# Performance work log

Measured on AMD Instinct MI355X. Metric: run time of the kernel, lower is better.

Reference implementation:

```python
import jax, jax.numpy as jnp
import numpy as np

H, KV, D = 12, 2, 128        # q heads, kv heads, head_dim
HID = 1536
B, S = 4, 2048               # equal-length packed sequences
T = B * S
EPS = 1e-6
ROPE_THETA = 10000.0


def _rms_norm(x, w):
    # RMSNorm over last dim in fp32, as in Qwen3RMSNorm
    xf = x.astype(jnp.float32)
    var = jnp.mean(xf * xf, axis=-1, keepdims=True)
    return (w * (xf * jax.lax.rsqrt(var + EPS))).astype(x.dtype)


def _apply_rope(x, cos, sin):
    # x: [T, h, D]; cos/sin: [T, D/2] -> expand over heads
    half = cos.shape[-1]
    x1, x2 = x[..., :half], x[..., half:2 * half]
    c = cos[:, None, :]
    s = sin[:, None, :]
    return jnp.concatenate([x1 * c - x2 * s, x1 * s + x2 * c], axis=-1)


def setup_inputs() -> dict:
    key = jax.random.key(0)
    ks = jax.random.split(key, 8)
    hidden_states = jax.random.normal(ks[0], (T, HID), dtype=jnp.float32)
    # real RoPE tables over per-sequence positions
    inv_freq = 1.0 / (ROPE_THETA ** (np.arange(0, D, 2, dtype=np.float32) / D))  # [D/2]
    pos = np.tile(np.arange(S, dtype=np.float32), B)                              # [T]
    ang = pos[:, None] * inv_freq[None, :]
    cos = jnp.asarray(np.cos(ang), dtype=jnp.float32)
    sin = jnp.asarray(np.sin(ang), dtype=jnp.float32)
    sc = 0.02
    Wq = jax.random.normal(ks[1], (HID, H * D), dtype=jnp.float32) * sc
    Wk = jax.random.normal(ks[2], (HID, KV * D), dtype=jnp.float32) * sc
    Wv = jax.random.normal(ks[3], (HID, KV * D), dtype=jnp.float32) * sc
    Wo = jax.random.normal(ks[4], (H * D, HID), dtype=jnp.float32) * sc
    q_norm_w = jnp.ones((D,), dtype=jnp.float32)
    k_norm_w = jnp.ones((D,), dtype=jnp.float32)
    cu_seqlens = jnp.arange(B + 1, dtype=jnp.int32) * S
    return {"hidden_states": hidden_states, "cos": cos, "sin": sin,
            "Wq": Wq, "Wk": Wk, "Wv": Wv, "Wo": Wo,
            "q_norm_w": q_norm_w, "k_norm_w": k_norm_w,
            "cu_seqlens": cu_seqlens}


def reference(hidden_states, cos, sin, Wq, Wk, Wv, Wo, q_norm_w, k_norm_w, cu_seqlens):
    # QKV projections on packed tokens
    q = (hidden_states @ Wq).reshape(T, H, D)
    k = (hidden_states @ Wk).reshape(T, KV, D)
    v = (hidden_states @ Wv).reshape(T, KV, D)
    # Qwen3 per-head QK RMSNorm, then RoPE
    q = _apply_rope(_rms_norm(q, q_norm_w), cos, sin)
    k = _apply_rope(_rms_norm(k, k_norm_w), cos, sin)
    # equal-length sequences: unpack to [B, h, S, D] (block-diagonal varlen attn)
    qb = q.reshape(B, S, H, D).transpose(0, 2, 1, 3)
    kb = k.reshape(B, S, KV, D).transpose(0, 2, 1, 3)
    vb = v.reshape(B, S, KV, D).transpose(0, 2, 1, 3)
    # GQA: repeat kv heads
    rep = H // KV
    kb = jnp.repeat(kb, rep, axis=1)
    vb = jnp.repeat(vb, rep, axis=1)
    scale = D ** -0.5
    scores = jnp.einsum('bhqd,bhkd->bhqk', qb, kb) * scale
    causal = jnp.tril(jnp.ones((S, S), dtype=bool))
    scores = jnp.where(causal[None, None], scores, jnp.finfo(scores.dtype).min)
    attn = jax.nn.softmax(scores, axis=-1)
    out = jnp.einsum('bhqk,bhkd->bhqd', attn, vb)       # [B,H,S,D]
    out = out.transpose(0, 2, 1, 3).reshape(T, H * D)   # repack
    return out @ Wo
```

## Files before the change

kernel.cpp:

```cpp
#include <hip/hip_runtime.h>
#include <hip/hip_bf16.h>
#include <stdint.h>

#define H_   12
#define KV_  2
#define D_   128
#define HID_ 1536
#define B_   4
#define S_   2048
#define T_   (B_*S_)

typedef __attribute__((ext_vector_type(8))) short  bf16x8;
typedef __attribute__((ext_vector_type(4))) float  f32x4;

__device__ __forceinline__ ushort f2bf(float f) {
  union { float f; uint32_t u; } v; v.f = f;
  uint32_t u = v.u;
  return (ushort)((u + 0x7fffu + ((u >> 16) & 1u)) >> 16);
}
__device__ __forceinline__ float bf2f(ushort u) {
  union { uint32_t u; float f; } v; v.u = ((uint32_t)u) << 16;
  return v.f;
}
__device__ __forceinline__ uint32_t cvtpk_bf16(float lo, float hi) {
  uint32_t r;
  asm("v_cvt_pk_bf16_f32 %0, %1, %2" : "=v"(r) : "v"(lo), "v"(hi));
  return r;
}

__device__ __forceinline__ void gload_lds16(const void* g, void* l) {
  __builtin_amdgcn_global_load_lds(
      (const __attribute__((address_space(1))) uint32_t*)g,
      (__attribute__((address_space(3))) uint32_t*)l, 16, 0, 0);
}

__global__ __launch_bounds__(256) void cvt_f32_bf16(const float* __restrict__ in,
                                                    ushort* __restrict__ out, int n) {
  int i = (blockIdx.x * 256 + threadIdx.x) * 4;
  if (i + 3 < n) {
    float4 v = *(const float4*)&in[i];
    ushort4 o;
    o.x = f2bf(v.x); o.y = f2bf(v.y); o.z = f2bf(v.z); o.w = f2bf(v.w);
    *(ushort4*)&out[i] = o;
  }
}

__global__ __launch_bounds__(256) void transpose_cvt2(const float* __restrict__ W0,
                                                      ushort* __restrict__ Wt0,
                                                      const float* __restrict__ W1,
                                                      ushort* __restrict__ Wt1,
                                                      int K, int N) {
  __shared__ float tile[32][33];
  const float* W  = blockIdx.z ? W1  : W0;
  ushort*      Wt = blockIdx.z ? Wt1 : Wt0;
  int k0 = blockIdx.x * 32, n0 = blockIdx.y * 32;
  int tx = threadIdx.x & 31, ty = threadIdx.x >> 5;
#pragma unroll
  for (int i = 0; i < 32; i += 8)
    tile[ty + i][tx] = W[(long)(k0 + ty + i) * N + n0 + tx];
  __syncthreads();
#pragma unroll
  for (int i = 0; i < 32; i += 8)
    Wt[(long)(n0 + ty + i) * K + k0 + tx] = f2bf(tile[tx][ty + i]);
}

template <int OUT_F32>
__global__ __launch_bounds__(256, 2) void gemm_bt(const ushort* __restrict__ A,
                                                  const ushort* __restrict__ Bt,
                                                  void* __restrict__ Cv,
                                                  int M, int N, int K, int lda) {
  __shared__ ushort lA[128 * 32];
  __shared__ ushort lB[128 * 32];
  const int tid = threadIdx.x;
  const int lane = tid & 63, w = tid >> 6;
  const int wr = w >> 1, wc = w & 1;
  const int l15 = lane & 15, lh = lane >> 4;
  const long m0 = (long)blockIdx.x * 128, n0 = (long)blockIdx.y * 128;
  const ushort* Ab = A + m0 * lda;
  const ushort* Bb = Bt + n0 * K;
  const int sr = tid >> 2;
  const int sc = (tid & 3) * 8;
  const int ldsoff = w * 512;
  f32x4 acc[4][4] = {};

  for (int k0 = 0; k0 < K; k0 += 32) {
#pragma unroll
    for (int it = 0; it < 2; ++it) {
      gload_lds16(Ab + (long)(it * 64 + sr) * lda + k0 + sc, &lA[it * 2048 + ldsoff]);
      gload_lds16(Bb + (long)(it * 64 + sr) * K + k0 + sc, &lB[it * 2048 + ldsoff]);
    }
    __syncthreads();
    bf16x8 af[4], bfr[4];
    const int ra = (wr * 64 + l15) * 32 + lh * 8;
    const int rb = (wc * 64 + l15) * 32 + lh * 8;
#pragma unroll
    for (int i = 0; i < 4; ++i) {
      af[i]  = *(const bf16x8*)&lA[ra + i * 16 * 32];
      bfr[i] = *(const bf16x8*)&lB[rb + i * 16 * 32];
    }
#pragma unroll
    for (int i = 0; i < 4; ++i)
#pragma unroll
      for (int j = 0; j < 4; ++j)
        acc[i][j] = __builtin_amdgcn_mfma_f32_16x16x32_bf16(af[i], bfr[j], acc[i][j], 0, 0, 0);
    __syncthreads();
  }
#pragma unroll
  for (int i = 0; i < 4; ++i) {
#pragma unroll
    for (int q = 0; q < 4; ++q) {
      long row = m0 + wr * 64 + i * 16 + lh * 4 + q;
#pragma unroll
      for (int j = 0; j < 4; ++j) {
        long col = n0 + wc * 64 + j * 16 + l15;
        float v = acc[i][j][q];
        if (OUT_F32) ((float*)Cv)[row * N + col] = v;
        else         ((ushort*)Cv)[row * N + col] = f2bf(v);
      }
    }
  }
}

template <int NH>
__global__ __launch_bounds__(256) void normrope(const ushort* __restrict__ X,
                                                int xstride,
                                                const float* __restrict__ w,
                                                const float* __restrict__ cosb,
                                                const float* __restrict__ sinb,
                                                ushort* __restrict__ Y,
                                                float scale) {
  int wid = (int)((blockIdx.x * 256 + threadIdx.x) >> 6);
  int lane = threadIdx.x & 63;
  if (wid >= T_ * NH) return;
  int t = wid / NH, h = wid % NH;
  const ushort* xr = X + (long)t * xstride + h * 128;
  float x1 = bf2f(xr[lane]);
  float x2 = bf2f(xr[lane + 64]);
  float ss = x1 * x1 + x2 * x2;
#pragma unroll
  for (int off = 32; off; off >>= 1) ss += __shfl_xor(ss, off);
  float r = rsqrtf(ss * (1.0f / 128.0f) + 1e-6f);
  float y1 = x1 * r * w[lane] * scale;
  float y2 = x2 * r * w[lane + 64] * scale;
  float c = cosb[(long)t * 64 + lane], s = sinb[(long)t * 64 + lane];
  float o1 = y1 * c - y2 * s;
  float o2 = y1 * s + y2 * c;
  int b = t / S_, sq = t % S_;
  ushort* yr = Y + ((long)(b * NH + h) * S_ + sq) * 128;
  yr[lane]      = f2bf(o1);
  yr[lane + 64] = f2bf(o2);
}

__global__ __launch_bounds__(256) void vtrans(const ushort* __restrict__ V, int vstride, int voff,
                                              ushort* __restrict__ Vt) {
  __shared__ ushort tile[32][33];
  int s0 = blockIdx.x * 32, d0 = blockIdx.y * 32;
  int bk = blockIdx.z;
  int b = bk / KV_, g = bk % KV_;
  int tx = threadIdx.x & 31, ty = threadIdx.x >> 5;
#pragma unroll
  for (int i = 0; i < 32; i += 8)
    tile[ty + i][tx] = V[(long)(b * S_ + s0 + ty + i) * vstride + voff + g * 128 + d0 + tx];
  __syncthreads();
#pragma unroll
  for (int i = 0; i < 32; i += 8)
    Vt[(long)(bk * 128 + d0 + ty + i) * S_ + s0 + tx] = tile[tx][ty + i];
}

__global__ __launch_bounds__(256, 2) void attn(ushort* __restrict__ QKV,
                                               const ushort* __restrict__ Ka,
                                               const ushort* __restrict__ Vt,
                                               const float* __restrict__ qnw,
                                               const float* __restrict__ cosb,
                                               const float* __restrict__ sinb) {
  __shared__ ushort lK[64 * 128];
  __shared__ ushort lV[128 * 64];
  __shared__ ushort lP[4 * 32 * 32];
  const int tid = threadIdx.x, lane = tid & 63, w = tid >> 6;
  const int l15 = lane & 15, lh = lane >> 4;
  char* cK = (char*)lK;
  char* cV = (char*)lV;
  char* cP = (char*)lP + w * 2048;
  const int swzK = l15 << 4;
  const int swzV = (l15 & 7) << 4;
  const int swzP = (l15 & 3) << 4;
  const float SCL = 0.08838834764831845f * 1.44269504088896f;
  const float M0  = 17.0f;

  const int qt = 15 - (int)(blockIdx.x / 48);
  const int bh = blockIdx.x % 48;
  const int b = bh / H_, h = bh % H_, g = h / (H_ / KV_);
  const int q0 = qt * 128;
  const ushort* Kb = Ka + (long)(b * KV_ + g) * S_ * 128;
  const ushort* Vb = Vt + (long)(b * KV_ + g) * 128 * S_;

  bf16x8 qf[2][4];
#pragma unroll
  for (int m = 0; m < 2; ++m) {
    const long tt = (long)b * S_ + q0 + w * 32 + m * 16 + l15;
    const ushort* xr = QKV + tt * 2048 + h * 128;
    bf16x8 raw[4];
#pragma unroll
    for (int kd = 0; kd < 4; ++kd)
      raw[kd] = *(const bf16x8*)&xr[kd * 32 + lh * 8];
    float ss = 0.f;
#pragma unroll
    for (int kd = 0; kd < 4; ++kd)
#pragma unroll
      for (int e = 0; e < 8; ++e) {
        float v = bf2f((ushort)raw[kd][e]);
        ss += v * v;
      }
    ss += __shfl_xor(ss, 16);
    ss += __shfl_xor(ss, 32);
    const float rn = rsqrtf(ss * (1.0f / 128.0f) + 1e-6f) * SCL;
    const float* cR = cosb + tt * 64;
    const float* sR = sinb + tt * 64;
#pragma unroll
    for (int kp = 0; kp < 2; ++kp) {
      bf16x8 qlo, qhi;
#pragma unroll
      for (int e = 0; e < 8; ++e) {
        const int ci = kp * 32 + lh * 8 + e;
        float c = cR[ci], s = sR[ci];
        float y1 = bf2f((ushort)raw[kp][e])     * rn * qnw[ci];
        float y2 = bf2f((ushort)raw[kp + 2][e]) * rn * qnw[64 + ci];
        qlo[e] = (short)f2bf(y1 * c - y2 * s);
        qhi[e] = (short)f2bf(y1 * s + y2 * c);
      }
      qf[m][kp]     = qlo;
      qf[m][kp + 2] = qhi;
    }
  }

  f32x4 o[2][8] = {};
  float lr[2] = {0.f, 0.f};
  const int nt = 2 * qt + 2;

  bf16x8 kreg[4], vreg[4];
#define LDTILE(K0) do { \
  _Pragma("unroll") for (int it = 0; it < 4; ++it) \
    kreg[it] = *(const bf16x8*)&Kb[(long)((K0) + it * 16 + (tid >> 4)) * 128 + (tid & 15) * 8]; \
  _Pragma("unroll") for (int it = 0; it < 4; ++it) \
    vreg[it] = *(const bf16x8*)&Vb[(long)(it * 32 + (tid >> 3)) * S_ + (K0) + (tid & 7) * 8]; \
} while (0)

  LDTILE(0);
  for (int t = 0; t < nt; ++t) {
    const int k0 = t * 64;
    __syncthreads();
#pragma unroll
    for (int it = 0; it < 4; ++it) {
      int r = it * 16 + (tid >> 4);
      *(bf16x8*)(cK + r * 256 + (((tid & 15) * 16) ^ (((tid >> 4) & 15) << 4))) = kreg[it];
    }
#pragma unroll
    for (int it = 0; it < 4; ++it) {
      int r = it * 32 + (tid >> 3);
      *(bf16x8*)(cV + r * 128 + (((tid & 7) * 16) ^ ((r & 7) << 4))) = vreg[it];
    }
    __syncthreads();
    if (t + 1 < nt) LDTILE(k0 + 64);

    if (k0 <= q0 + w * 32 + 31) {
      f32x4 sfr[2][4] = {};
      __builtin_amdgcn_s_setprio(1);
#pragma unroll
      for (int kd = 0; kd < 4; ++kd) {
        bf16x8 kf[4];
#pragma unroll
        for (int n = 0; n < 4; ++n)
          kf[n] = *(const bf16x8*)(cK + (n * 16 + l15) * 256 + ((kd * 64 + lh * 16) ^ swzK));
#pragma unroll
        for (int m = 0; m < 2; ++m)
#pragma unroll
          for (int n = 0; n < 4; ++n)
            sfr[m][n] = __builtin_amdgcn_mfma_f32_16x16x32_bf16(kf[n], qf[m][kd], sfr[m][n], 0, 0, 0);
      }
      __builtin_amdgcn_s_setprio(0);
      const bool boundary = (k0 + 63 > q0 + w * 32);
      if (boundary) {
#pragma unroll
        for (int m = 0; m < 2; ++m) {
          const int rowm = q0 + w * 32 + m * 16 + l15;
#pragma unroll
          for (int n = 0; n < 4; ++n) {
            int kb = k0 + n * 16 + lh * 4;
#pragma unroll
            for (int qr = 0; qr < 4; ++qr)
              if (kb + qr > rowm) sfr[m][n][qr] = -INFINITY;
          }
        }
      }
#pragma unroll
      for (int m = 0; m < 2; ++m) {
#pragma unroll
        for (int n = 0; n < 4; ++n) {
          float p0 = exp2f(sfr[m][n][0] - M0);
          float p1 = exp2f(sfr[m][n][1] - M0);
          float p2 = exp2f(sfr[m][n][2] - M0);
          float p3 = exp2f(sfr[m][n][3] - M0);
          sfr[m][n][0] = p0; sfr[m][n][1] = p1; sfr[m][n][2] = p2; sfr[m][n][3] = p3;
          lr[m] += (p0 + p1) + (p2 + p3);
        }
      }
#pragma unroll
      for (int kf2 = 0; kf2 < 2; ++kf2) {
#pragma unroll
        for (int m = 0; m < 2; ++m)
#pragma unroll
          for (int nl = 0; nl < 2; ++nl) {
            const int n = kf2 * 2 + nl;
            uint2 pk;
            pk.x = cvtpk_bf16(sfr[m][n][0], sfr[m][n][1]);
            pk.y = cvtpk_bf16(sfr[m][n][2], sfr[m][n][3]);
            *(uint2*)(cP + (m * 16 + l15) * 64 + ((nl * 32 + lh * 8) ^ swzP)) = pk;
          }
        const int cb = (lh * 16) ^ swzP;
        bf16x8 pf0 = *(const bf16x8*)(cP + l15 * 64 + cb);
        bf16x8 pf1 = *(const bf16x8*)(cP + (16 + l15) * 64 + cb);
        const int cv = (kf2 * 64 + lh * 16);
        __builtin_amdgcn_s_setprio(1);
#pragma unroll
        for (int dblk = 0; dblk < 8; ++dblk) {
          bf16x8 vf = *(const bf16x8*)(cV + (dblk * 16 + l15) * 128 + (cv ^ swzV));
          o[0][dblk] = __builtin_amdgcn_mfma_f32_16x16x32_bf16(pf0, vf, o[0][dblk], 0, 0, 0);
          o[1][dblk] = __builtin_amdgcn_mfma_f32_16x16x32_bf16(pf1, vf, o[1][dblk], 0, 0, 0);
        }
        __builtin_amdgcn_s_setprio(0);
      }
    }
  }
#undef LDTILE
#pragma unroll
  for (int m = 0; m < 2; ++m) {
    lr[m] += __shfl_xor(lr[m], 16);
    lr[m] += __shfl_xor(lr[m], 32);
    float inv = 1.f / lr[m];
#pragma unroll
    for (int qr = 0; qr < 4; ++qr) {
      float iv = __shfl(inv, lh * 4 + qr);
      long trow = (long)b * S_ + q0 + w * 32 + m * 16 + lh * 4 + qr;
#pragma unroll
      for (int dblk = 0; dblk < 8; ++dblk)
        QKV[trow * 2048 + h * 128 + dblk * 16 + l15] = f2bf(o[m][dblk][qr] * iv);
    }
  }
}

extern "C" void kernel_launch(void* const* d_in, const int* in_sizes, int n_in,
                              void* d_out, int out_size, void* d_ws, size_t ws_size,
                              hipStream_t stream) {
  const float* hs   = (const float*)d_in[0];
  const float* cosb = (const float*)d_in[1];
  const float* sinb = (const float*)d_in[2];
  const float* Wq   = (const float*)d_in[3];
  const float* Wk   = (const float*)d_in[4];
  const float* Wv   = (const float*)d_in[5];
  const float* Wo   = (const float*)d_in[6];
  const float* qw   = (const float*)d_in[7];
  const float* kw   = (const float*)d_in[8];
  (void)in_sizes; (void)n_in; (void)out_size; (void)ws_size;

  char* ws = (char*)d_ws;
  size_t off = 0;
  auto alloc = [&](size_t bytes) {
    void* p = ws + off;
    off += (bytes + 255) & ~(size_t)255;
    return p;
  };
  ushort* Xb  = (ushort*)alloc((size_t)T_ * HID_ * 2);
  ushort* Wqt = (ushort*)alloc((size_t)HID_ * HID_ * 2);
  ushort* Wkt = (ushort*)alloc((size_t)256 * HID_ * 2);
  ushort* Wvt = (ushort*)alloc((size_t)256 * HID_ * 2);
  ushort* Wot = (ushort*)alloc((size_t)HID_ * HID_ * 2);
  ushort* qkv = (ushort*)alloc((size_t)T_ * 2048 * 2);
  ushort* ka  = (ushort*)alloc((size_t)T_ * 256 * 2);
  ushort* vt  = (ushort*)alloc((size_t)T_ * 256 * 2);

  cvt_f32_bf16<<<(T_ * HID_ / 4 + 255) / 256, 256, 0, stream>>>(hs, Xb, T_ * HID_);
  transpose_cvt2<<<dim3(HID_ / 32, HID_ / 32, 2), 256, 0, stream>>>(Wq, Wqt, Wo, Wot, HID_, HID_);
  transpose_cvt2<<<dim3(HID_ / 32, 256 / 32, 2), 256, 0, stream>>>(Wk, Wkt, Wv, Wvt, HID_, 256);

  gemm_bt<0><<<dim3(T_ / 128, 2048 / 128), 256, 0, stream>>>(Xb, Wqt, qkv, T_, 2048, HID_, HID_);

  normrope<KV_><<<(T_ * KV_ + 3) / 4, 256, 0, stream>>>(qkv + 1536, 2048, kw, cosb, sinb, ka, 1.0f);
  vtrans<<<dim3(S_ / 32, 128 / 32, B_ * KV_), 256, 0, stream>>>(qkv, 2048, 1792, vt);

  attn<<<768, 256, 0, stream>>>(qkv, ka, vt, qw, cosb, sinb);

  gemm_bt<1><<<dim3(T_ / 128, 1536 / 128), 256, 0, stream>>>(qkv, Wot, (float*)d_out, T_, 1536, HID_, 2048);
}
```

Baseline: 229.2 us.

## Use 256x256 double-buffered GEMM tile for the QKV projection

Adds a new GEMM kernel with 256x256 output tiles, 512 threads, K-step 64, double-buffered LDS with direct global-to-LDS loads, an XOR swizzle, and raised wave priority around the MFMA loop. The QKV projection now uses it in place of the 128x128 kernel, to get more operand reuse per LDS load and to overlap the next tile's loads with compute. In exchange it uses much more LDS and registers (128 KB LDS, 32 accumulators per lane), which lowers occupancy, and it launches only 256 blocks on a large-CU device, which may leave some compute units idle.

```diff
diff --git a/kernel.cpp b/kernel.cpp
--- a/kernel.cpp
+++ b/kernel.cpp
@@ -114,6 +114,85 @@
       for (int j = 0; j < 4; ++j) {
         long col = n0 + wc * 64 + j * 16 + l15;
         float v = acc[i][j][q];
+        if (OUT_F32) ((float*)Cv)[row * N + col] = v;
+        else         ((ushort*)Cv)[row * N + col] = f2bf(v);
+      }
+    }
+  }
+}
+
+template <int OUT_F32>
+__global__ __launch_bounds__(512) void gemm256(const ushort* __restrict__ A,
+                                               const ushort* __restrict__ Bt,
+                                               void* __restrict__ Cv,
+                                               int M, int N, int K, int lda) {
+  __shared__ ushort lA[2][256 * 64];
+  __shared__ ushort lB[2][256 * 64];
+  const int tid = threadIdx.x, lane = tid & 63;
+  const int w = tid >> 6;
+  const int l15 = lane & 15, lh = lane >> 4;
+  const int wr = w >> 2, wc = w & 3;
+  const long m0 = (long)blockIdx.x * 256, n0 = (long)blockIdx.y * 256;
+  const ushort* Ab = A + m0 * lda;
+  const ushort* Bb = Bt + n0 * K;
+  const int swz = (l15 & 7) << 4;
+
+  f32x4 acc[8][4] = {};
+  const int NT = K / 64;
+
+#define STAGE256(KT, PB) do {                                                      \
+  const int k0s = (KT) * 64;                                                       \
+  _Pragma("unroll") for (int it = 0; it < 4; ++it) {                               \
+    int ch = it * 512 + tid; int r = ch >> 3, s = ch & 7;                          \
+    int cb = it * 512 + (tid & 448);                                               \
+    gload_lds16(Ab + (long)r * lda + k0s + ((s ^ (r & 7)) * 8), &lA[PB][cb * 8]);  \
+  }                                                                                \
+  _Pragma("unroll") for (int it = 0; it < 4; ++it) {                               \
+    int ch = it * 512 + tid; int r = ch >> 3, s = ch & 7;                          \
+    int cb = it * 512 + (tid & 448);                                               \
+    gload_lds16(Bb + (long)r * K + k0s + ((s ^ (r & 7)) * 8), &lB[PB][cb * 8]);    \
+  }                                                                                \
+} while (0)
+
+  STAGE256(0, 0);
+  __syncthreads();
+  int p = 0;
+  for (int kt = 0; kt < NT; ++kt) {
+    if (kt + 1 < NT) STAGE256(kt + 1, p ^ 1);
+    const char* cA = (const char*)&lA[p][0];
+    const char* cB = (const char*)&lB[p][0];
+    bf16x8 bf[4][2];
+#pragma unroll
+    for (int fj = 0; fj < 4; ++fj)
+#pragma unroll
+      for (int kk = 0; kk < 2; ++kk)
+        bf[fj][kk] = *(const bf16x8*)(cB + (wc * 64 + fj * 16 + l15) * 128 + ((kk * 64 + lh * 16) ^ swz));
+    __builtin_amdgcn_s_setprio(1);
+#pragma unroll
+    for (int fi = 0; fi < 8; ++fi) {
+      const int ra = (wr * 128 + fi * 16 + l15) * 128;
+      bf16x8 af0 = *(const bf16x8*)(cA + ra + ((lh * 16) ^ swz));
+      bf16x8 af1 = *(const bf16x8*)(cA + ra + ((64 + lh * 16) ^ swz));
+#pragma unroll
+      for (int fj = 0; fj < 4; ++fj) {
+        acc[fi][fj] = __builtin_amdgcn_mfma_f32_16x16x32_bf16(af0, bf[fj][0], acc[fi][fj], 0, 0, 0);
+        acc[fi][fj] = __builtin_amdgcn_mfma_f32_16x16x32_bf16(af1, bf[fj][1], acc[fi][fj], 0, 0, 0);
+      }
+    }
+    __builtin_amdgcn_s_setprio(0);
+    __syncthreads();
+    p ^= 1;
+  }
+#undef STAGE256
+#pragma unroll
+  for (int fi = 0; fi < 8; ++fi) {
+#pragma unroll
+    for (int q = 0; q < 4; ++q) {
+      long row = m0 + wr * 128 + fi * 16 + lh * 4 + q;
+#pragma unroll
+      for (int fj = 0; fj < 4; ++fj) {
+        long col = n0 + wc * 64 + fj * 16 + l15;
+        float v = acc[fi][fj][q];
         if (OUT_F32) ((float*)Cv)[row * N + col] = v;
         else         ((ushort*)Cv)[row * N + col] = f2bf(v);
       }
@@ -382,7 +461,7 @@
   transpose_cvt2<<<dim3(HID_ / 32, HID_ / 32, 2), 256, 0, stream>>>(Wq, Wqt, Wo, Wot, HID_, HID_);
   transpose_cvt2<<<dim3(HID_ / 32, 256 / 32, 2), 256, 0, stream>>>(Wk, Wkt, Wv, Wvt, HID_, 256);
 
-  gemm_bt<0><<<dim3(T_ / 128, 2048 / 128), 256, 0, stream>>>(Xb, Wqt, qkv, T_, 2048, HID_, HID_);
+  gemm256<0><<<dim3(T_ / 256, 2048 / 256), 512, 0, stream>>>(Xb, Wqt, qkv, T_, 2048, HID_, HID_);
 
   normrope<KV_><<<(T_ * KV_ + 3) / 4, 256, 0, stream>>>(qkv + 1536, 2048, kw, cosb, sinb, ka, 1.0f);
   vtrans<<<dim3(S_ / 32, 128 / 32, B_ * KV_), 256, 0, stream>>>(qkv, 2048, 1792, vt);
```

Measured after the change: 215.9 us. -5.8%, faster.
